# Optimization experiments

Measured on AMD Instinct MI355X. Metric: run time of the kernel, lower is better.

## Reference

```python
import jax, jax.numpy as jnp
import numpy as np

B, T, D, E, TOP_K = 8, 2048, 512, 8, 2


def setup_inputs() -> dict:
    key = jax.random.key(0)
    ks = jax.random.split(key, 8)
    s = 0.02
    return {
        "x": jax.random.normal(ks[0], (B, T, D), dtype=jnp.float32),
        "eps": jax.random.normal(ks[1], (B, T, E), dtype=jnp.float32),
        "Wr": jax.random.normal(ks[2], (D, E), dtype=jnp.float32) * s,
        "br": jnp.zeros((E,), dtype=jnp.float32),
        "Wn": jax.random.normal(ks[3], (D, E), dtype=jnp.float32) * s,
        "bn": jnp.zeros((E,), dtype=jnp.float32),
        "Wk": jax.random.normal(ks[4], (E, D, D), dtype=jnp.float32) * s,
        "bk": jnp.zeros((E, D), dtype=jnp.float32),
    }


def reference(x, eps, Wr, br, Wn, bn, Wk, bk):
    # Noisy top-k router (NoisyTopkRouter.forward)
    logits = jnp.einsum("btd,de->bte", x, Wr) + br            # [B,T,E]
    noise_logits = jnp.einsum("btd,de->bte", x, Wn) + bn      # [B,T,E]
    noisy = logits + eps * jax.nn.softplus(noise_logits)      # [B,T,E]
    _, top_idx = jax.lax.top_k(noisy, TOP_K)                  # [B,T,k]
    # mask[b,t,e] = True iff expert e is in the token's top-k
    topk_mask = jax.nn.one_hot(top_idx, E, dtype=jnp.float32).sum(-2) > 0
    sparse_logits = jnp.where(topk_mask, noisy, -jnp.inf)
    gating = jax.nn.softmax(sparse_logits, axis=-1)           # zero for non-top-k experts
    # Dense dispatch: every expert's Linear applied to all tokens, then
    # gating (zero outside top-k) selects/scales — same math as the masked
    # gather + per-expert Linear + gating scale in SparseMoE.forward.
    expert_out = jnp.einsum("btd,edh->bteh", x, Wk) + bk      # [B,T,E,D]
    out = jnp.einsum("bte,bteh->bth", gating, expert_out)     # [B,T,D]
    return out
```

## Files before the change

### kernel.cpp

```cpp
#include <hip/hip_runtime.h>
#include <hip/hip_bf16.h>
#include <math.h>

#define B_    8
#define T_    2048
#define NTOK  (B_ * T_)
#define D_    512
#define E_    8
#define CAP   NTOK

#define RV_TOK    32
#define RV_THR    256
#define XS_STRIDE 132
#define WS_FLOATS 2108

typedef __attribute__((ext_vector_type(4))) float f32x4;
typedef __attribute__((ext_vector_type(8))) short short8;

__device__ __forceinline__ void async_load16(const void* g, void* l) {
    __builtin_amdgcn_global_load_lds(
        (const __attribute__((address_space(1))) unsigned int*)g,
        (__attribute__((address_space(3))) unsigned int*)l,
        16, 0, 0);
}

__global__ __launch_bounds__(256) void transpose_wk(
    const float* __restrict__ Wk, __hip_bfloat16* __restrict__ Wkt)
{
    __shared__ float tile[32][33];
    const int e  = blockIdx.z;
    const int d0 = blockIdx.x * 32;
    const int h0 = blockIdx.y * 32;
    const int tx = threadIdx.x, ty = threadIdx.y;

    const float* src = Wk + ((size_t)e * D_ + d0) * D_ + h0;
    #pragma unroll
    for (int r = ty; r < 32; r += 8)
        tile[r][tx] = src[(size_t)r * D_ + tx];
    __syncthreads();
    __hip_bfloat16* dst = Wkt + ((size_t)e * D_ + h0) * D_ + d0;
    #pragma unroll
    for (int r = ty; r < 32; r += 8)
        dst[(size_t)r * D_ + tx] = __float2bfloat16(tile[tx][r]);
}

__global__ __launch_bounds__(RV_THR) void router_kernel(
    const float* __restrict__ x,
    const float* __restrict__ eps,
    const float* __restrict__ Wr,
    const float* __restrict__ br,
    const float* __restrict__ Wn,
    const float* __restrict__ bn,
    __hip_bfloat16* __restrict__ xb,
    uint4* __restrict__ top2)
{
    __shared__ float xs[RV_TOK * XS_STRIDE];
    __shared__ float wsh[WS_FLOATS];

    const int tid  = threadIdx.x;
    const int tok0 = blockIdx.x * RV_TOK;
    const int lane = tid & 63, wv = tid >> 6;
    const int kidx = lane >> 2, ts = lane & 3;
    const int ta = wv * 8 + ts, tb = ta + 4;
    const int wk = tid >> 1, wh = tid & 1;

    float accA[16], accB[16];
    #pragma unroll
    for (int c = 0; c < 16; ++c) { accA[c] = 0.f; accB[c] = 0.f; }

    for (int kc = 0; kc < D_; kc += 128) {
        #pragma unroll
        for (int it = 0; it < 4; ++it) {
            const int f   = it * RV_THR + tid;
            const int row = f >> 5, col = (f & 31) * 4;
            const f32x4 v = *(const f32x4*)(x + (size_t)(tok0 + row) * D_ + kc + col);
            *(f32x4*)(xs + row * XS_STRIDE + col) = v;
            union { __hip_bfloat16 h[4]; uint2 u; } cv;
            cv.h[0] = __float2bfloat16(v.x); cv.h[1] = __float2bfloat16(v.y);
            cv.h[2] = __float2bfloat16(v.z); cv.h[3] = __float2bfloat16(v.w);
            *(uint2*)(xb + (size_t)(tok0 + row) * D_ + kc + col) = cv.u;
        }
        {
            const float* src = (wh ? Wn : Wr) + (size_t)(kc + wk) * E_;
            const f32x4 w0 = *(const f32x4*)(src);
            const f32x4 w1 = *(const f32x4*)(src + 4);
            float* dst = wsh + wk * 16 + (wk >> 3) * 4 + wh * 8;
            *(f32x4*)(dst)     = w0;
            *(f32x4*)(dst + 4) = w1;
        }
        __syncthreads();

        const float* xra = xs + ta * XS_STRIDE + kidx * 8;
        const float* xrb = xs + tb * XS_STRIDE + kidx * 8;
        const f32x4 xa0 = *(const f32x4*)(xra);
        const f32x4 xa1 = *(const f32x4*)(xra + 4);
        const f32x4 xc0 = *(const f32x4*)(xrb);
        const f32x4 xc1 = *(const f32x4*)(xrb + 4);
        const float* wbase = wsh + kidx * 132;
        #pragma unroll
        for (int kk = 0; kk < 8; ++kk) {
            const float xav = (kk < 4) ? xa0[kk] : xa1[kk - 4];
            const float xbv = (kk < 4) ? xc0[kk] : xc1[kk - 4];
            const float* wrow = wbase + kk * 16;
            #pragma unroll
            for (int c4 = 0; c4 < 4; ++c4) {
                const f32x4 w = *(const f32x4*)(wrow + c4 * 4);
                #pragma unroll
                for (int c = 0; c < 4; ++c) {
                    accA[c4 * 4 + c] = fmaf(xav, w[c], accA[c4 * 4 + c]);
                    accB[c4 * 4 + c] = fmaf(xbv, w[c], accB[c4 * 4 + c]);
                }
            }
        }
        __syncthreads();
    }

    #pragma unroll
    for (int off = 4; off < 64; off <<= 1) {
        #pragma unroll
        for (int c = 0; c < 16; ++c) {
            accA[c] += __shfl_xor(accA[c], off);
            accB[c] += __shfl_xor(accB[c], off);
        }
    }

    if (lane < 4) {
        #pragma unroll
        for (int half = 0; half < 2; ++half) {
            const int tok = tok0 + (half ? tb : ta);
            float nv[8];
            #pragma unroll
            for (int e = 0; e < 8; ++e) {
                const float rd = half ? accB[e] : accA[e];
                const float nd = half ? accB[8 + e] : accA[8 + e];
                const float nl = nd + bn[e];
                const float sp = fmaxf(nl, 0.f) + log1pf(expf(-fabsf(nl)));
                nv[e] = rd + br[e] + eps[(size_t)tok * E_ + e] * sp;
            }
            int i1 = 0; float v1 = nv[0];
            #pragma unroll
            for (int e = 1; e < 8; ++e)
                if (nv[e] > v1) { v1 = nv[e]; i1 = e; }
            int i2 = -1; float v2 = -3.4e38f;
            #pragma unroll
            for (int e = 0; e < 8; ++e)
                if (e != i1 && nv[e] > v2) { v2 = nv[e]; i2 = e; }
            const float t  = expf(v2 - v1);
            const float g1 = 1.f / (1.f + t);
            const float g2 = t / (1.f + t);
            top2[tok] = make_uint4((unsigned)i1 | ((unsigned)i2 << 8),
                                   __float_as_uint(g1), __float_as_uint(g2), 0u);
        }
    }
}

__global__ __launch_bounds__(256) void bucket_kernel(
    const uint4* __restrict__ top2,
    int* __restrict__ counts,
    uint2* __restrict__ entries)
{
    __shared__ int hist[E_];
    __shared__ int base[E_];
    const int tid = threadIdx.x;
    const int tok = blockIdx.x * 256 + tid;
    if (tid < E_) hist[tid] = 0;
    __syncthreads();
    const uint4 t = top2[tok];
    const int i1 = t.x & 0xff, i2 = (t.x >> 8) & 0xff;
    const int l1 = atomicAdd(&hist[i1], 1);
    const int l2 = atomicAdd(&hist[i2], 1);
    __syncthreads();
    if (tid < E_) base[tid] = atomicAdd(counts + tid, hist[tid]);
    __syncthreads();
    entries[(size_t)i1 * CAP + base[i1] + l1] = make_uint2((unsigned)tok, t.y);
    entries[(size_t)i2 * CAP + base[i2] + l2] =
        make_uint2((unsigned)tok | 0x80000000u, t.z);
}

__global__ __launch_bounds__(256) void moe_gemm(
    const __hip_bfloat16* __restrict__ xb,
    const __hip_bfloat16* __restrict__ wkt,
    const float* __restrict__ bk,
    const int* __restrict__ counts,
    const uint2* __restrict__ entries,
    __hip_bfloat16* __restrict__ outg,
    float* __restrict__ out,
    int use_slots)
{
    constexpr int BM = 128, BN = 128, BK = 32;
    __shared__ __hip_bfloat16 As[BM * BK];
    __shared__ __hip_bfloat16 Bs[BN * BK];
    __shared__ uint2 ent[BM];

    const int e  = blockIdx.z;
    const int mt = blockIdx.y;
    const int nt = blockIdx.x;
    const int cnt = counts[e];
    if (mt * BM >= cnt) return;

    const int tid = threadIdx.x;
    const int wave = tid >> 6, lane = tid & 63;

    if (tid < BM) {
        const int idx = mt * BM + tid;
        ent[tid] = (idx < cnt) ? entries[(size_t)e * CAP + idx] : make_uint2(0u, 0u);
    }
    __syncthreads();

    const int quad = lane >> 4, lr = lane & 15;
    const int wm = wave >> 1, wn = wave & 1;
    const int sub = lane >> 2, part = lane & 3;

    f32x4 acc[4][4];
    #pragma unroll
    for (int i = 0; i < 4; ++i)
        #pragma unroll
        for (int j = 0; j < 4; ++j) acc[i][j] = (f32x4){0.f, 0.f, 0.f, 0.f};

    const size_t tok0 = ent[wave * 32 + sub].x & 0x7fffffffu;
    const size_t tok1 = ent[wave * 32 + 16 + sub].x & 0x7fffffffu;
    const size_t brow0 = (size_t)e * D_ + nt * BN + wave * 32 + sub;

    for (int k0 = 0; k0 < D_; k0 += BK) {
        async_load16(xb + tok0 * D_ + k0 + part * 8, As + (wave * 32) * BK);
        async_load16(xb + tok1 * D_ + k0 + part * 8, As + (wave * 32 + 16) * BK);
        async_load16(wkt + brow0 * D_ + k0 + part * 8, Bs + (wave * 32) * BK);
        async_load16(wkt + (brow0 + 16) * D_ + k0 + part * 8, Bs + (wave * 32 + 16) * BK);
        __syncthreads();

        short8 a[4], b[4];
        #pragma unroll
        for (int i = 0; i < 4; ++i)
            a[i] = *(const short8*)(As + (wm * 64 + i * 16 + lr) * BK + quad * 8);
        #pragma unroll
        for (int j = 0; j < 4; ++j)
            b[j] = *(const short8*)(Bs + (wn * 64 + j * 16 + lr) * BK + quad * 8);
        #pragma unroll
        for (int i = 0; i < 4; ++i)
            #pragma unroll
            for (int j = 0; j < 4; ++j)
                acc[i][j] = __builtin_amdgcn_mfma_f32_16x16x32_bf16(a[i], b[j], acc[i][j], 0, 0, 0);
        __syncthreads();
    }

    const int colbase = nt * BN + wn * 64 + lr;
    float bkv[4];
    #pragma unroll
    for (int j = 0; j < 4; ++j) bkv[j] = bk[e * D_ + colbase + j * 16];

    #pragma unroll
    for (int i = 0; i < 4; ++i) {
        #pragma unroll
        for (int r = 0; r < 4; ++r) {
            const int row = wm * 64 + i * 16 + quad * 4 + r;
            if (mt * BM + row < cnt) {
                const uint2 en = ent[row];
                const unsigned ts2 = en.x;
                const float g = __uint_as_float(en.y);
                if (use_slots) {
                    __hip_bfloat16* orow = outg + ((size_t)(ts2 >> 31) * NTOK
                                          + (ts2 & 0x7fffffffu)) * D_ + colbase;
                    #pragma unroll
                    for (int j = 0; j < 4; ++j)
                        orow[j * 16] = __float2bfloat16(g * (acc[i][j][r] + bkv[j]));
                } else {
                    float* orow = out + (size_t)(ts2 & 0x7fffffffu) * D_ + colbase;
                    #pragma unroll
                    for (int j = 0; j < 4; ++j)
                        atomicAdd(orow + j * 16, g * (acc[i][j][r] + bkv[j]));
                }
            }
        }
    }
}

__global__ __launch_bounds__(256) void combine_kernel(
    const __hip_bfloat16* __restrict__ outg, float* __restrict__ out)
{
    const size_t i = ((size_t)blockIdx.x * 256 + threadIdx.x) * 8;
    const uint4 u0 = *(const uint4*)(outg + i);
    const uint4 u1 = *(const uint4*)(outg + (size_t)NTOK * D_ + i);
    const unsigned* a = (const unsigned*)&u0;
    const unsigned* b = (const unsigned*)&u1;
    float o[8];
    #pragma unroll
    for (int k = 0; k < 4; ++k) {
        o[2*k]   = __uint_as_float(a[k] << 16) + __uint_as_float(b[k] << 16);
        o[2*k+1] = __uint_as_float(a[k] & 0xffff0000u)
                 + __uint_as_float(b[k] & 0xffff0000u);
    }
    *(f32x4*)(out + i)     = *(f32x4*)(o);
    *(f32x4*)(out + i + 4) = *(f32x4*)(o + 4);
}

extern "C" void kernel_launch(void* const* d_in, const int* in_sizes, int n_in,
                              void* d_out, int out_size, void* d_ws, size_t ws_size,
                              hipStream_t stream) {
    const float* x   = (const float*)d_in[0];
    const float* eps = (const float*)d_in[1];
    const float* Wr  = (const float*)d_in[2];
    const float* br  = (const float*)d_in[3];
    const float* Wn  = (const float*)d_in[4];
    const float* bn  = (const float*)d_in[5];
    const float* Wk  = (const float*)d_in[6];
    const float* bk  = (const float*)d_in[7];
    float* out = (float*)d_out;

    char* ws = (char*)d_ws;
    size_t off = 0;
    int* counts = (int*)(ws + off);                     off += 256;
    uint2* entries = (uint2*)(ws + off);                off += (size_t)E_ * CAP * 8;
    __hip_bfloat16* xb = (__hip_bfloat16*)(ws + off);   off += (size_t)NTOK * D_ * 2;
    __hip_bfloat16* wkt = (__hip_bfloat16*)(ws + off);  off += (size_t)E_ * D_ * D_ * 2;
    uint4* top2 = (uint4*)(ws + off);                   off += (size_t)NTOK * 16;
    __hip_bfloat16* outg = (__hip_bfloat16*)(ws + off); off += (size_t)2 * NTOK * D_ * 2;
    const int use_slots = (ws_size >= off) ? 1 : 0;

    hipMemsetAsync(counts, 0, E_ * sizeof(int), stream);
    if (!use_slots)
        hipMemsetAsync(out, 0, (size_t)out_size * sizeof(float), stream);

    transpose_wk<<<dim3(16, 16, E_), dim3(32, 8), 0, stream>>>(Wk, wkt);
    router_kernel<<<dim3(NTOK / RV_TOK), dim3(RV_THR), 0, stream>>>(
        x, eps, Wr, br, Wn, bn, xb, top2);
    bucket_kernel<<<dim3(NTOK / 256), dim3(256), 0, stream>>>(top2, counts, entries);
    moe_gemm<<<dim3(D_ / 128, CAP / 128, E_), dim3(256), 0, stream>>>(
        xb, wkt, bk, counts, entries, outg, out, use_slots);
    if (use_slots)
        combine_kernel<<<dim3((NTOK * D_) / (256 * 8)), dim3(256), 0, stream>>>(outg, out);
}
```

Measured before the change: 175.9 us.

## Widen MoE GEMM N-tile to 256 and halve router tokens per block

The MoE expert GEMM now uses a 128x256 output tile, so each wave computes 4x8 MFMA tiles and loads four B rows per k-step. This halves the number of N blocks and reuses each gathered A tile across twice as many columns, cutting redundant gathers of token rows. The cost is doubled accumulator registers, with launch_bounds(256,2) asking for two blocks per CU. Separately, the router processes 16 tokens per block with one token per thread, which doubles the block count for more parallelism but spreads each weight load over fewer tokens.

```diff
diff --git a/kernel.cpp b/kernel.cpp
--- a/kernel.cpp
+++ b/kernel.cpp
@@ -9,7 +9,7 @@
 #define E_    8
 #define CAP   NTOK
 
-#define RV_TOK    32
+#define RV_TOK    16
 #define RV_THR    256
 #define XS_STRIDE 132
 #define WS_FLOATS 2108
@@ -61,16 +61,16 @@
     const int tok0 = blockIdx.x * RV_TOK;
     const int lane = tid & 63, wv = tid >> 6;
     const int kidx = lane >> 2, ts = lane & 3;
-    const int ta = wv * 8 + ts, tb = ta + 4;
+    const int tl = wv * 4 + ts;
     const int wk = tid >> 1, wh = tid & 1;
 
-    float accA[16], accB[16];
-    #pragma unroll
-    for (int c = 0; c < 16; ++c) { accA[c] = 0.f; accB[c] = 0.f; }
+    float acc[16];
+    #pragma unroll
+    for (int c = 0; c < 16; ++c) acc[c] = 0.f;
 
     for (int kc = 0; kc < D_; kc += 128) {
         #pragma unroll
-        for (int it = 0; it < 4; ++it) {
+        for (int it = 0; it < 2; ++it) {
             const int f   = it * RV_THR + tid;
             const int row = f >> 5, col = (f & 31) * 4;
             const f32x4 v = *(const f32x4*)(x + (size_t)(tok0 + row) * D_ + kc + col);
@@ -90,26 +90,20 @@
         }
         __syncthreads();
 
-        const float* xra = xs + ta * XS_STRIDE + kidx * 8;
-        const float* xrb = xs + tb * XS_STRIDE + kidx * 8;
+        const float* xra = xs + tl * XS_STRIDE + kidx * 8;
         const f32x4 xa0 = *(const f32x4*)(xra);
         const f32x4 xa1 = *(const f32x4*)(xra + 4);
-        const f32x4 xc0 = *(const f32x4*)(xrb);
-        const f32x4 xc1 = *(const f32x4*)(xrb + 4);
         const float* wbase = wsh + kidx * 132;
         #pragma unroll
         for (int kk = 0; kk < 8; ++kk) {
             const float xav = (kk < 4) ? xa0[kk] : xa1[kk - 4];
-            const float xbv = (kk < 4) ? xc0[kk] : xc1[kk - 4];
             const float* wrow = wbase + kk * 16;
             #pragma unroll
             for (int c4 = 0; c4 < 4; ++c4) {
                 const f32x4 w = *(const f32x4*)(wrow + c4 * 4);
                 #pragma unroll
-                for (int c = 0; c < 4; ++c) {
-                    accA[c4 * 4 + c] = fmaf(xav, w[c], accA[c4 * 4 + c]);
-                    accB[c4 * 4 + c] = fmaf(xbv, w[c], accB[c4 * 4 + c]);
-                }
+                for (int c = 0; c < 4; ++c)
+                    acc[c4 * 4 + c] = fmaf(xav, w[c], acc[c4 * 4 + c]);
             }
         }
         __syncthreads();
@@ -118,39 +112,32 @@
     #pragma unroll
     for (int off = 4; off < 64; off <<= 1) {
         #pragma unroll
-        for (int c = 0; c < 16; ++c) {
-            accA[c] += __shfl_xor(accA[c], off);
-            accB[c] += __shfl_xor(accB[c], off);
-        }
+        for (int c = 0; c < 16; ++c)
+            acc[c] += __shfl_xor(acc[c], off);
     }
 
     if (lane < 4) {
-        #pragma unroll
-        for (int half = 0; half < 2; ++half) {
-            const int tok = tok0 + (half ? tb : ta);
-            float nv[8];
-            #pragma unroll
-            for (int e = 0; e < 8; ++e) {
-                const float rd = half ? accB[e] : accA[e];
-                const float nd = half ? accB[8 + e] : accA[8 + e];
-                const float nl = nd + bn[e];
-                const float sp = fmaxf(nl, 0.f) + log1pf(expf(-fabsf(nl)));
-                nv[e] = rd + br[e] + eps[(size_t)tok * E_ + e] * sp;
-            }
-            int i1 = 0; float v1 = nv[0];
-            #pragma unroll
-            for (int e = 1; e < 8; ++e)
-                if (nv[e] > v1) { v1 = nv[e]; i1 = e; }
-            int i2 = -1; float v2 = -3.4e38f;
-            #pragma unroll
-            for (int e = 0; e < 8; ++e)
-                if (e != i1 && nv[e] > v2) { v2 = nv[e]; i2 = e; }
-            const float t  = expf(v2 - v1);
-            const float g1 = 1.f / (1.f + t);
-            const float g2 = t / (1.f + t);
-            top2[tok] = make_uint4((unsigned)i1 | ((unsigned)i2 << 8),
-                                   __float_as_uint(g1), __float_as_uint(g2), 0u);
-        }
+        const int tok = tok0 + tl;
+        float nv[8];
+        #pragma unroll
+        for (int e = 0; e < 8; ++e) {
+            const float nl = acc[8 + e] + bn[e];
+            const float sp = fmaxf(nl, 0.f) + log1pf(expf(-fabsf(nl)));
+            nv[e] = acc[e] + br[e] + eps[(size_t)tok * E_ + e] * sp;
+        }
+        int i1 = 0; float v1 = nv[0];
+        #pragma unroll
+        for (int e = 1; e < 8; ++e)
+            if (nv[e] > v1) { v1 = nv[e]; i1 = e; }
+        int i2 = -1; float v2 = -3.4e38f;
+        #pragma unroll
+        for (int e = 0; e < 8; ++e)
+            if (e != i1 && nv[e] > v2) { v2 = nv[e]; i2 = e; }
+        const float t  = expf(v2 - v1);
+        const float g1 = 1.f / (1.f + t);
+        const float g2 = t / (1.f + t);
+        top2[tok] = make_uint4((unsigned)i1 | ((unsigned)i2 << 8),
+                               __float_as_uint(g1), __float_as_uint(g2), 0u);
     }
 }
 
@@ -177,7 +164,7 @@
         make_uint2((unsigned)tok | 0x80000000u, t.z);
 }
 
-__global__ __launch_bounds__(256) void moe_gemm(
+__global__ __launch_bounds__(256, 2) void moe_gemm(
     const __hip_bfloat16* __restrict__ xb,
     const __hip_bfloat16* __restrict__ wkt,
     const float* __restrict__ bk,
@@ -187,7 +174,7 @@
     float* __restrict__ out,
     int use_slots)
 {
-    constexpr int BM = 128, BN = 128, BK = 32;
+    constexpr int BM = 128, BN = 256, BK = 32;
     __shared__ __hip_bfloat16 As[BM * BK];
     __shared__ __hip_bfloat16 Bs[BN * BK];
     __shared__ uint2 ent[BM];
@@ -211,42 +198,44 @@
     const int wm = wave >> 1, wn = wave & 1;
     const int sub = lane >> 2, part = lane & 3;
 
-    f32x4 acc[4][4];
+    f32x4 acc[4][8];
     #pragma unroll
     for (int i = 0; i < 4; ++i)
         #pragma unroll
-        for (int j = 0; j < 4; ++j) acc[i][j] = (f32x4){0.f, 0.f, 0.f, 0.f};
+        for (int j = 0; j < 8; ++j) acc[i][j] = (f32x4){0.f, 0.f, 0.f, 0.f};
 
     const size_t tok0 = ent[wave * 32 + sub].x & 0x7fffffffu;
     const size_t tok1 = ent[wave * 32 + 16 + sub].x & 0x7fffffffu;
-    const size_t brow0 = (size_t)e * D_ + nt * BN + wave * 32 + sub;
+    const size_t brow0 = (size_t)e * D_ + nt * BN + wave * 64 + sub;
 
     for (int k0 = 0; k0 < D_; k0 += BK) {
         async_load16(xb + tok0 * D_ + k0 + part * 8, As + (wave * 32) * BK);
         async_load16(xb + tok1 * D_ + k0 + part * 8, As + (wave * 32 + 16) * BK);
-        async_load16(wkt + brow0 * D_ + k0 + part * 8, Bs + (wave * 32) * BK);
-        async_load16(wkt + (brow0 + 16) * D_ + k0 + part * 8, Bs + (wave * 32 + 16) * BK);
+        #pragma unroll
+        for (int q = 0; q < 4; ++q)
+            async_load16(wkt + (brow0 + q * 16) * D_ + k0 + part * 8,
+                         Bs + (wave * 64 + q * 16) * BK);
         __syncthreads();
 
-        short8 a[4], b[4];
+        short8 a[4], b[8];
         #pragma unroll
         for (int i = 0; i < 4; ++i)
             a[i] = *(const short8*)(As + (wm * 64 + i * 16 + lr) * BK + quad * 8);
         #pragma unroll
-        for (int j = 0; j < 4; ++j)
-            b[j] = *(const short8*)(Bs + (wn * 64 + j * 16 + lr) * BK + quad * 8);
+        for (int j = 0; j < 8; ++j)
+            b[j] = *(const short8*)(Bs + (wn * 128 + j * 16 + lr) * BK + quad * 8);
         #pragma unroll
         for (int i = 0; i < 4; ++i)
             #pragma unroll
-            for (int j = 0; j < 4; ++j)
+            for (int j = 0; j < 8; ++j)
                 acc[i][j] = __builtin_amdgcn_mfma_f32_16x16x32_bf16(a[i], b[j], acc[i][j], 0, 0, 0);
         __syncthreads();
     }
 
-    const int colbase = nt * BN + wn * 64 + lr;
-    float bkv[4];
-    #pragma unroll
-    for (int j = 0; j < 4; ++j) bkv[j] = bk[e * D_ + colbase + j * 16];
+    const int colbase = nt * BN + wn * 128 + lr;
+    float bkv[8];
+    #pragma unroll
+    for (int j = 0; j < 8; ++j) bkv[j] = bk[e * D_ + colbase + j * 16];
 
     #pragma unroll
     for (int i = 0; i < 4; ++i) {
@@ -261,12 +250,12 @@
                     __hip_bfloat16* orow = outg + ((size_t)(ts2 >> 31) * NTOK
                                           + (ts2 & 0x7fffffffu)) * D_ + colbase;
                     #pragma unroll
-                    for (int j = 0; j < 4; ++j)
+                    for (int j = 0; j < 8; ++j)
                         orow[j * 16] = __float2bfloat16(g * (acc[i][j][r] + bkv[j]));
                 } else {
                     float* orow = out + (size_t)(ts2 & 0x7fffffffu) * D_ + colbase;
                     #pragma unroll
-                    for (int j = 0; j < 4; ++j)
+                    for (int j = 0; j < 8; ++j)
                         atomicAdd(orow + j * 16, g * (acc[i][j][r] + bkv[j]));
                 }
             }
@@ -324,7 +313,7 @@
     router_kernel<<<dim3(NTOK / RV_TOK), dim3(RV_THR), 0, stream>>>(
         x, eps, Wr, br, Wn, bn, xb, top2);
     bucket_kernel<<<dim3(NTOK / 256), dim3(256), 0, stream>>>(top2, counts, entries);
-    moe_gemm<<<dim3(D_ / 128, CAP / 128, E_), dim3(256), 0, stream>>>(
+    moe_gemm<<<dim3(D_ / 256, CAP / 128, E_), dim3(256), 0, stream>>>(
         xb, wkt, bk, counts, entries, outg, out, use_slots);
     if (use_slots)
         combine_kernel<<<dim3((NTOK * D_) / (256 * 8)), dim3(256), 0, stream>>>(outg, out);
```

After: 177.0 us. About the same (+0.6%).
